# Kernel tuning notes

Measured on AMD Instinct MI355X. Metric: run time of the kernel, lower is better.

Reference implementation:

```python
import jax, jax.numpy as jnp
import numpy as np

N = 50000      # nodes
E = 800000     # edges
IN = 128       # in_dim
EMB = 32       # emb_dim
ED = 8         # edge_dim
L = 4          # num_layers
B = 64         # num graphs in batch
OUT = 10       # out_dim
EPS = 1e-5


def setup_inputs() -> dict:
    key = jax.random.key(0)
    ks = jax.random.split(key, 16)
    f32 = jnp.float32
    def nrm(k, shape, scale):
        return jax.random.normal(k, shape, dtype=f32) * scale
    inp = {}
    inp['x'] = nrm(ks[0], (N, IN), 1.0)
    inp['edge_index'] = jax.random.randint(ks[1], (2, E), 0, N)
    inp['edge_attr'] = nrm(ks[2], (E, ED), 1.0)
    inp['batch'] = jnp.sort(jax.random.randint(ks[3], (N,), 0, B))
    # lin_in
    inp['lin_in_w'] = nrm(ks[4], (IN, EMB), 0.05)
    inp['lin_in_b'] = jnp.zeros((EMB,), f32)
    # per-layer message MLP: Linear(2e+ed->e), BN, ReLU, Linear(e->e), BN, ReLU
    inp['msg_w1'] = nrm(ks[5], (L, 2 * EMB + ED, EMB), 0.1)
    inp['msg_b1'] = jnp.zeros((L, EMB), f32)
    inp['msg_g1'] = jnp.ones((L, EMB), f32)
    inp['msg_be1'] = jnp.zeros((L, EMB), f32)
    inp['msg_w2'] = nrm(ks[6], (L, EMB, EMB), 0.1)
    inp['msg_b2'] = jnp.zeros((L, EMB), f32)
    inp['msg_g2'] = jnp.ones((L, EMB), f32)
    inp['msg_be2'] = jnp.zeros((L, EMB), f32)
    # per-layer update MLP: Linear(2e->e), BN, ReLU, Linear(e->e), BN, ReLU
    inp['upd_w1'] = nrm(ks[7], (L, 2 * EMB, EMB), 0.1)
    inp['upd_b1'] = jnp.zeros((L, EMB), f32)
    inp['upd_g1'] = jnp.ones((L, EMB), f32)
    inp['upd_be1'] = jnp.zeros((L, EMB), f32)
    inp['upd_w2'] = nrm(ks[8], (L, EMB, EMB), 0.1)
    inp['upd_b2'] = jnp.zeros((L, EMB), f32)
    inp['upd_g2'] = jnp.ones((L, EMB), f32)
    inp['upd_be2'] = jnp.zeros((L, EMB), f32)
    # lin_pred
    inp['pred_w'] = nrm(ks[9], (EMB, OUT), 0.1)
    inp['pred_b'] = jnp.zeros((OUT,), f32)
    return inp


def _bn(x, g, b):
    # BatchNorm1d in training mode: batch stats over dim 0 (biased variance)
    mu = jnp.mean(x, axis=0)
    var = jnp.mean(jnp.square(x - mu), axis=0)
    return (x - mu) * jax.lax.rsqrt(var + EPS) * g + b


def reference(x, edge_attr, lin_in_w, lin_in_b,
              msg_w1, msg_b1, msg_g1, msg_be1, msg_w2, msg_b2, msg_g2, msg_be2,
              upd_w1, upd_b1, upd_g1, upd_be1, upd_w2, upd_b2, upd_g2, upd_be2,
              pred_w, pred_b, edge_index, batch):
    src = edge_index[0]  # h_j source nodes
    dst = edge_index[1]  # h_i target nodes (aggregation index)
    h = x @ lin_in_w + lin_in_b  # [N, EMB]
    for i in range(L):
        # message: gather + concat + MLP(BN,ReLU)x2 over edges
        msg_in = jnp.concatenate([h[dst], h[src], edge_attr], axis=-1)  # [E, 2e+ed]
        m = jax.nn.relu(_bn(msg_in @ msg_w1[i] + msg_b1[i], msg_g1[i], msg_be1[i]))
        m = jax.nn.relu(_bn(m @ msg_w2[i] + msg_b2[i], msg_g2[i], msg_be2[i]))
        # aggregate: scatter-add by destination
        aggr = jax.ops.segment_sum(m, dst, num_segments=N)  # [N, EMB]
        # update: concat + MLP(BN,ReLU)x2
        u = jnp.concatenate([h, aggr], axis=-1)  # [N, 2e]
        u = jax.nn.relu(_bn(u @ upd_w1[i] + upd_b1[i], upd_g1[i], upd_be1[i]))
        u = jax.nn.relu(_bn(u @ upd_w2[i] + upd_b2[i], upd_g2[i], upd_be2[i]))
        h = u + h  # residual in MPNNModel.get_embeddings
    # global mean pool
    sums = jax.ops.segment_sum(h, batch, num_segments=B)
    counts = jax.ops.segment_sum(jnp.ones((N,), h.dtype), batch, num_segments=B)
    h_graph = sums / jnp.maximum(counts, 1.0)[:, None]
    return h_graph @ pred_w + pred_b  # [B, OUT]
```

## Files before the change

### kernel.cpp

```cpp
#include <hip/hip_runtime.h>
#include <cstddef>

#define N_NODES 50000
#define N_EDGES 800000
#define IN_DIM  128
#define EMB     32
#define ED      8
#define NLAYERS 4
#define NB      64
#define OUTD    10
#define EPS_BN  1e-5f

#define EDGE_GRID 3125
#define NODE_GRID 196
#define NODE4_GRID 782
#define AU_GRID   6250
#define NT16      50000
#define NTILE_N   3125
#define LIN_GRID  782
#define MSG2_TPW  16
#define MSG2_GRID 782

#define SREP 4

typedef short bf16x8 __attribute__((ext_vector_type(8)));
typedef float f32x4  __attribute__((ext_vector_type(4)));


__device__ __forceinline__ unsigned short f2bf(float x) {
  union { float f; unsigned u; } v; v.f = x;
  unsigned b = v.u + 0x7FFFu + ((v.u >> 16) & 1u);
  return (unsigned short)(b >> 16);
}
__device__ __forceinline__ float bf2f(unsigned short s) {
  union { unsigned u; float f; } v; v.u = ((unsigned)s) << 16;
  return v.f;
}

__device__ __forceinline__ void coef_from_stats(const float* __restrict__ stats_stage,
                                                const float* __restrict__ g,
                                                const float* __restrict__ be,
                                                float inv_count, float* __restrict__ cf) {
  if (threadIdx.x < EMB) {
    const int c = threadIdx.x;
    float s = 0.f, ss = 0.f;
#pragma unroll
    for (int r = 0; r < SREP; ++r) {
      s  += stats_stage[r*64 + c];
      ss += stats_stage[r*64 + EMB + c];
    }
    const float mu  = s * inv_count;
    const float var = ss * inv_count - mu*mu;
    const float a = g[c] * rsqrtf(var + EPS_BN);
    cf[c] = a;
    cf[EMB + c] = fmaf(-mu, a, be[c]);
  }
  __syncthreads();
}

__device__ __forceinline__ void wave_stats_atomic(float ts[8], float tss[8],
                                                  float* __restrict__ lds_s,
                                                  float* __restrict__ lds_q,
                                                  float* __restrict__ stats_stage) {
  const int lane = threadIdx.x & 63;
  const int wv   = threadIdx.x >> 6;
#pragma unroll
  for (int j = 0; j < 8; ++j) {
    float a = ts[j], b = tss[j];
#pragma unroll
    for (int o = 32; o > 0; o >>= 1) {
      a += __shfl_down(a, o, 64);
      b += __shfl_down(b, o, 64);
    }
    ts[j] = a; tss[j] = b;
  }
  if (lane == 0) {
#pragma unroll
    for (int j = 0; j < 8; ++j) {
      lds_s[wv*8 + j] = ts[j];
      lds_q[wv*8 + j] = tss[j];
    }
  }
  __syncthreads();
  if (threadIdx.x < 64) {
    const float v = (threadIdx.x < 32) ? lds_s[threadIdx.x] : lds_q[threadIdx.x - 32];
    atomicAdd(stats_stage + ((blockIdx.x & (SREP-1)) << 6) + threadIdx.x, v);
  }
}

__device__ __forceinline__ void half_stats_atomic(const float ts[16], const float tss[16],
                                                  float* __restrict__ stats_stage) {
  __shared__ float s_s[4][32], s_q[4][32];
  const int lane = threadIdx.x & 63;
  const int wid  = threadIdx.x >> 6;
#pragma unroll
  for (int j = 0; j < 16; ++j) {
    float a = ts[j], q = tss[j];
#pragma unroll
    for (int o = 32; o >= 2; o >>= 1) {
      a += __shfl_down(a, o, 64);
      q += __shfl_down(q, o, 64);
    }
    if (lane < 2) { s_s[wid][lane*16 + j] = a; s_q[wid][lane*16 + j] = q; }
  }
  __syncthreads();
  if (threadIdx.x < 64) {
    const int c = threadIdx.x & 31;
    const int kind = threadIdx.x >> 5;
    float v = 0.f;
#pragma unroll
    for (int wq = 0; wq < 4; ++wq)
      v += kind ? s_q[wq][c] : s_s[wq][c];
    atomicAdd(stats_stage + ((blockIdx.x & (SREP-1)) << 6) + kind*32 + c, v);
  }
}

#define HSTRIDE 40

__global__ __launch_bounds__(256) void k_lin_in_pq(
    const float* __restrict__ x, const float* __restrict__ w, const float* __restrict__ b,
    const float* __restrict__ w1, const float* __restrict__ b1, const int* __restrict__ ei,
    float* __restrict__ h, unsigned short* __restrict__ p, unsigned short* __restrict__ q,
    int* __restrict__ cnt)
{
  __shared__ __align__(16) unsigned short lds_hb[4][16*HSTRIDE];
  __shared__ __align__(16) unsigned short lds_pq[4][16*HSTRIDE];
  const int lane = threadIdx.x & 63;
  const int wv   = threadIdx.x >> 6;
  const int n0i  = lane & 15;
  const int quad = lane >> 4;

  const int tile = blockIdx.x*4 + wv;
  if (tile < NTILE_N) {
    const int r0 = tile*16;
    bf16x8 BwL[4], BwH[4];
#pragma unroll
    for (int kb = 0; kb < 4; ++kb) {
#pragma unroll
      for (int j = 0; j < 8; ++j) {
        const int k = kb*32 + quad*8 + j;
        BwL[kb][j] = (short)f2bf(w[k*EMB + n0i]);
        BwH[kb][j] = (short)f2bf(w[k*EMB + 16 + n0i]);
      }
    }
    f32x4 accL = {0.f,0.f,0.f,0.f};
    f32x4 accH = {0.f,0.f,0.f,0.f};
#pragma unroll
    for (int kb = 0; kb < 4; ++kb) {
      const float4 xa = *(const float4*)(x + (size_t)(r0 + n0i)*IN_DIM + kb*32 + quad*8);
      const float4 xb = *(const float4*)(x + (size_t)(r0 + n0i)*IN_DIM + kb*32 + quad*8 + 4);
      bf16x8 A;
      A[0] = (short)f2bf(xa.x); A[1] = (short)f2bf(xa.y);
      A[2] = (short)f2bf(xa.z); A[3] = (short)f2bf(xa.w);
      A[4] = (short)f2bf(xb.x); A[5] = (short)f2bf(xb.y);
      A[6] = (short)f2bf(xb.z); A[7] = (short)f2bf(xb.w);
      accL = __builtin_amdgcn_mfma_f32_16x16x32_bf16(A, BwL[kb], accL, 0, 0, 0);
      accH = __builtin_amdgcn_mfma_f32_16x16x32_bf16(A, BwH[kb], accH, 0, 0, 0);
    }
    const float bL = b[n0i], bH = b[16 + n0i];
#pragma unroll
    for (int r = 0; r < 4; ++r) {
      const int row = quad*4 + r;
      const float vL = accL[r] + bL;
      const float vH = accH[r] + bH;
      h[(size_t)(r0 + row)*EMB + n0i]      = vL;
      h[(size_t)(r0 + row)*EMB + 16 + n0i] = vH;
      lds_hb[wv][row*HSTRIDE + n0i]      = f2bf(vL);
      lds_hb[wv][row*HSTRIDE + 16 + n0i] = f2bf(vH);
    }
    bf16x8 A2;
#pragma unroll
    for (int j = 0; j < 8; ++j)
      A2[j] = (short)lds_hb[wv][n0i*HSTRIDE + quad*8 + j];
    bf16x8 BpL, BpH, BqL, BqH;
#pragma unroll
    for (int j = 0; j < 8; ++j) {
      const int k = quad*8 + j;
      BpL[j] = (short)f2bf(w1[k*EMB + n0i]);
      BpH[j] = (short)f2bf(w1[k*EMB + 16 + n0i]);
      BqL[j] = (short)f2bf(w1[(EMB + k)*EMB + n0i]);
      BqH[j] = (short)f2bf(w1[(EMB + k)*EMB + 16 + n0i]);
    }
    const f32x4 z4 = {0.f,0.f,0.f,0.f};
    f32x4 pL = __builtin_amdgcn_mfma_f32_16x16x32_bf16(A2, BpL, z4, 0, 0, 0);
    f32x4 pH = __builtin_amdgcn_mfma_f32_16x16x32_bf16(A2, BpH, z4, 0, 0, 0);
    f32x4 qL = __builtin_amdgcn_mfma_f32_16x16x32_bf16(A2, BqL, z4, 0, 0, 0);
    f32x4 qH = __builtin_amdgcn_mfma_f32_16x16x32_bf16(A2, BqH, z4, 0, 0, 0);
    const float b1L = b1[n0i], b1H = b1[16 + n0i];
#pragma unroll
    for (int r = 0; r < 4; ++r) {
      const int row = quad*4 + r;
      lds_pq[wv][row*HSTRIDE + n0i]      = f2bf(pL[r] + b1L);
      lds_pq[wv][row*HSTRIDE + 16 + n0i] = f2bf(pH[r] + b1H);
    }
    {
      const int row2 = lane >> 2;
      const int c8   = (lane & 3)*8;
      const uint4 ov = *(const uint4*)&lds_pq[wv][row2*HSTRIDE + c8];
      *(uint4*)(p + (size_t)(r0 + row2)*EMB + c8) = ov;
    }
#pragma unroll
    for (int r = 0; r < 4; ++r) {
      const int row = quad*4 + r;
      lds_pq[wv][row*HSTRIDE + n0i]      = f2bf(qL[r]);
      lds_pq[wv][row*HSTRIDE + 16 + n0i] = f2bf(qH[r]);
    }
    {
      const int row2 = lane >> 2;
      const int c8   = (lane & 3)*8;
      const uint4 ov = *(const uint4*)&lds_pq[wv][row2*HSTRIDE + c8];
      *(uint4*)(q + (size_t)(r0 + row2)*EMB + c8) = ov;
    }
  }
  for (int e = blockIdx.x*256 + threadIdx.x; e < N_EDGES; e += gridDim.x*256)
    atomicAdd(&cnt[ei[N_EDGES + e]], 1);
}

__global__ __launch_bounds__(256) void k_scan_a(const int* __restrict__ cnt,
                                                int* __restrict__ row_ptr, int* __restrict__ bsum) {
  __shared__ int s[256];
  const int gid = blockIdx.x*256 + threadIdx.x;
  const int v = (gid < N_NODES) ? cnt[gid] : 0;
  s[threadIdx.x] = v;
  __syncthreads();
  for (int o = 1; o < 256; o <<= 1) {
    const int t = (threadIdx.x >= o) ? s[threadIdx.x - o] : 0;
    __syncthreads();
    s[threadIdx.x] += t;
    __syncthreads();
  }
  if (gid < N_NODES) row_ptr[gid] = s[threadIdx.x] - v;
  if (threadIdx.x == 255) bsum[blockIdx.x] = s[255];
}

__global__ __launch_bounds__(256) void k_scan_bc(int* __restrict__ row_ptr,
                                                 const int* __restrict__ bsum) {
  __shared__ int s[256];
  const int t = threadIdx.x;
  const int v = (t < NODE_GRID) ? bsum[t] : 0;
  s[t] = v;
  __syncthreads();
  for (int o = 1; o < 256; o <<= 1) {
    const int tt = (t >= o) ? s[t - o] : 0;
    __syncthreads();
    s[t] += tt;
    __syncthreads();
  }
  const int off = (blockIdx.x == 0) ? 0 : s[blockIdx.x - 1];
  const int gid = blockIdx.x*256 + t;
  if (gid < N_NODES) row_ptr[gid] += off;
  if (blockIdx.x == 0 && t == 0) row_ptr[N_NODES] = N_EDGES;
}

__global__ __launch_bounds__(256) void k_place_scatter(
    const int* __restrict__ ei, const float* __restrict__ ea,
    const int* __restrict__ row_ptr, int* __restrict__ cnt2,
    uint2* __restrict__ rec)
{
  const int e = blockIdx.x*256 + threadIdx.x;
  const int s = ei[e];
  const int d = ei[N_EDGES + e];
  const int pos = row_ptr[d] + atomicAdd(&cnt2[d], 1);
  const float4 v0 = ((const float4*)(ea + (size_t)e*ED))[0];
  const float4 v1 = ((const float4*)(ea + (size_t)e*ED))[1];
  const float ev[8] = {v0.x, v0.y, v0.z, v0.w, v1.x, v1.y, v1.z, v1.w};
  unsigned u[4];
#pragma unroll
  for (int j = 0; j < 4; ++j)
    u[j] = (unsigned)f2bf(ev[2*j]) | ((unsigned)f2bf(ev[2*j+1]) << 16);
  uint2* rp = rec + (size_t)pos*3;
  rp[0] = make_uint2((unsigned)s, (unsigned)d);
  rp[1] = make_uint2(u[0], u[1]);
  rp[2] = make_uint2(u[2], u[3]);
}


__device__ __forceinline__ void msg1_edge(const uint4 Pa, const uint4 Pb,
                                          const uint4 Qa, const uint4 Qb,
                                          const uint2 rb, const uint2 rc,
                                          const float* __restrict__ wh,
                                          float acc[16])
{
  const unsigned pw[8] = {Pa.x,Pa.y,Pa.z,Pa.w,Pb.x,Pb.y,Pb.z,Pb.w};
  const unsigned qw[8] = {Qa.x,Qa.y,Qa.z,Qa.w,Qb.x,Qb.y,Qb.z,Qb.w};
#pragma unroll
  for (int t = 0; t < 8; ++t) {
    acc[2*t]   = bf2f((unsigned short)(pw[t] & 0xFFFFu)) +
                 bf2f((unsigned short)(qw[t] & 0xFFFFu));
    acc[2*t+1] = bf2f((unsigned short)(pw[t] >> 16)) +
                 bf2f((unsigned short)(qw[t] >> 16));
  }
  const unsigned ew[4] = {rb.x, rb.y, rc.x, rc.y};
  float ev[8];
#pragma unroll
  for (int t = 0; t < 4; ++t) {
    ev[2*t]   = bf2f((unsigned short)(ew[t] & 0xFFFFu));
    ev[2*t+1] = bf2f((unsigned short)(ew[t] >> 16));
  }
#pragma unroll
  for (int k = 0; k < 8; ++k) {
    const float* wk = wh + k*EMB;
#pragma unroll
    for (int j = 0; j < 16; ++j) acc[j] = fmaf(ev[k], wk[j], acc[j]);
  }
}

__device__ __forceinline__ void msg1_store_stats(const float acc[16],
                                                 unsigned short* __restrict__ dst,
                                                 float ts[16], float tss[16])
{
  unsigned u[8];
#pragma unroll
  for (int j = 0; j < 8; ++j) {
    const unsigned short l0 = f2bf(acc[2*j]);
    const unsigned short h0 = f2bf(acc[2*j+1]);
    u[j] = (unsigned)l0 | ((unsigned)h0 << 16);
    const float v0 = bf2f(l0), v1 = bf2f(h0);
    ts[2*j]   += v0; tss[2*j]   = fmaf(v0, v0, tss[2*j]);
    ts[2*j+1] += v1; tss[2*j+1] = fmaf(v1, v1, tss[2*j+1]);
  }
  uint4 o0; o0.x = u[0]; o0.y = u[1]; o0.z = u[2]; o0.w = u[3];
  uint4 o1; o1.x = u[4]; o1.y = u[5]; o1.z = u[6]; o1.w = u[7];
  ((uint4*)dst)[0] = o0;
  ((uint4*)dst)[1] = o1;
}

__global__ __launch_bounds__(256) void k_msg1(
    const unsigned short* __restrict__ pb, const unsigned short* __restrict__ qb,
    const uint2* __restrict__ rec, const float* __restrict__ w1b,
    unsigned short* __restrict__ y, float* __restrict__ stats)
{
  const int t    = threadIdx.x;
  const int half = t & 1;
  const int eh   = t >> 1;
  const int e0   = blockIdx.x*256 + eh;
  const int e1   = e0 + 128;

  const uint2 r0a = rec[(size_t)e0*3];
  const uint2 r0b = rec[(size_t)e0*3 + 1];
  const uint2 r0c = rec[(size_t)e0*3 + 2];
  const uint2 r1a = rec[(size_t)e1*3];
  const uint2 r1b = rec[(size_t)e1*3 + 1];
  const uint2 r1c = rec[(size_t)e1*3 + 2];

  const uint4* p0 = (const uint4*)(pb + (size_t)r0a.y * EMB) + half*2;
  const uint4* q0 = (const uint4*)(qb + (size_t)r0a.x * EMB) + half*2;
  const uint4* p1 = (const uint4*)(pb + (size_t)r1a.y * EMB) + half*2;
  const uint4* q1 = (const uint4*)(qb + (size_t)r1a.x * EMB) + half*2;
  const uint4 P0a = p0[0], P0b = p0[1];
  const uint4 Q0a = q0[0], Q0b = q0[1];
  const uint4 P1a = p1[0], P1b = p1[1];
  const uint4 Q1a = q1[0], Q1b = q1[1];

  const float* wh = w1b + half*16;

  float ts[16], tss[16];
#pragma unroll
  for (int j = 0; j < 16; ++j) { ts[j] = 0.f; tss[j] = 0.f; }

  float acc[16];
  msg1_edge(P0a, P0b, Q0a, Q0b, r0b, r0c, wh, acc);
  msg1_store_stats(acc, y + (size_t)e0*EMB + half*16, ts, tss);
  msg1_edge(P1a, P1b, Q1a, Q1b, r1b, r1c, wh, acc);
  msg1_store_stats(acc, y + (size_t)e1*EMB + half*16, ts, tss);

  half_stats_atomic(ts, tss, stats);
}

__global__ __launch_bounds__(256) void k_msg2(
    unsigned short* __restrict__ y,
    const float* __restrict__ stats1, const float* __restrict__ g1, const float* __restrict__ be1,
    const float* __restrict__ w2, const float* __restrict__ b2,
    float* __restrict__ stats2)
{
  __shared__ __align__(16) unsigned short lds_t[4][16*32];
  __shared__ float lds_s[4][32], lds_q[4][32];
  __shared__ float cf[64];

  coef_from_stats(stats1, g1, be1, 1.0f/(float)N_EDGES, cf);

  const int lane = threadIdx.x & 63;
  const int wid  = threadIdx.x >> 6;
  const int n0 = lane & 15;
  const int kb = lane >> 4;

  bf16x8 Blo, Bhi;
#pragma unroll
  for (int j = 0; j < 8; ++j) {
    Blo[j] = (short)f2bf(w2[(kb*8 + j)*EMB + n0]);
    Bhi[j] = (short)f2bf(w2[(kb*8 + j)*EMB + 16 + n0]);
  }
  float a1[8], c1[8];
#pragma unroll
  for (int j = 0; j < 8; ++j) {
    a1[j] = cf[kb*8 + j];
    c1[j] = cf[EMB + kb*8 + j];
  }
  const float b2c0 = b2[n0], b2c1 = b2[16 + n0];

  float ts[8], tss[8];
#pragma unroll
  for (int j = 0; j < 8; ++j) { ts[j] = 0.f; tss[j] = 0.f; }

  const int tile0 = blockIdx.x * (MSG2_TPW*4);
  for (int t = 0; t < MSG2_TPW; ++t) {
    const int tile = tile0 + t*4 + wid;
    if (tile >= NT16) break;
    const size_t e0 = (size_t)tile * 16;

    const uint4 araw = *(const uint4*)(y + (e0 + n0)*EMB + kb*8);
    unsigned int ua[4] = {araw.x, araw.y, araw.z, araw.w};
    bf16x8 A;
#pragma unroll
    for (int j = 0; j < 4; ++j) {
      float v0 = bf2f((unsigned short)(ua[j] & 0xFFFFu));
      float v1 = bf2f((unsigned short)(ua[j] >> 16));
      v0 = fmaxf(fmaf(a1[2*j],   v0, c1[2*j]),   0.f);
      v1 = fmaxf(fmaf(a1[2*j+1], v1, c1[2*j+1]), 0.f);
      A[2*j]   = (short)f2bf(v0);
      A[2*j+1] = (short)f2bf(v1);
    }

    f32x4 acc0 = {0.f, 0.f, 0.f, 0.f};
    f32x4 acc1 = {0.f, 0.f, 0.f, 0.f};
    acc0 = __builtin_amdgcn_mfma_f32_16x16x32_bf16(A, Blo, acc0, 0, 0, 0);
    acc1 = __builtin_amdgcn_mfma_f32_16x16x32_bf16(A, Bhi, acc1, 0, 0, 0);

#pragma unroll
    for (int r = 0; r < 4; ++r) {
      const int row = kb*4 + r;
      lds_t[wid][row*32 + n0]      = f2bf(acc0[r] + b2c0);
      lds_t[wid][row*32 + 16 + n0] = f2bf(acc1[r] + b2c1);
    }
    const uint4 orow = *(const uint4*)&lds_t[wid][(lane>>2)*32 + (lane&3)*8];
    *(uint4*)(y + (e0 + (lane>>2))*EMB + (lane&3)*8) = orow;

    unsigned int uo[4] = {orow.x, orow.y, orow.z, orow.w};
#pragma unroll
    for (int j = 0; j < 4; ++j) {
      const float v0 = bf2f((unsigned short)(uo[j] & 0xFFFFu));
      const float v1 = bf2f((unsigned short)(uo[j] >> 16));
      ts[2*j]   += v0;  tss[2*j]   = fmaf(v0, v0, tss[2*j]);
      ts[2*j+1] += v1;  tss[2*j+1] = fmaf(v1, v1, tss[2*j+1]);
    }
  }

#pragma unroll
  for (int j = 0; j < 8; ++j) {
    float s = ts[j], qq = tss[j];
#pragma unroll
    for (int o = 4; o < 64; o <<= 1) {
      s  += __shfl_xor(s, o, 64);
      qq += __shfl_xor(qq, o, 64);
    }
    ts[j] = s; tss[j] = qq;
  }
  if (lane < 4) {
#pragma unroll
    for (int j = 0; j < 8; ++j) {
      lds_s[wid][lane*8 + j] = ts[j];
      lds_q[wid][lane*8 + j] = tss[j];
    }
  }
  __syncthreads();
  if (threadIdx.x < 64) {
    const int c = threadIdx.x & 31;
    const int kind = threadIdx.x >> 5;
    float v = 0.f;
#pragma unroll
    for (int wq = 0; wq < 4; ++wq)
      v += kind ? lds_q[wq][c] : lds_s[wq][c];
    atomicAdd(stats2 + ((blockIdx.x & (SREP-1)) << 6) + kind*32 + c, v);
  }
}

__global__ __launch_bounds__(256) void k_aggr_upd1(
    const unsigned short* __restrict__ y, const int* __restrict__ row_ptr,
    const float* __restrict__ h,
    const float* __restrict__ stats1, const float* __restrict__ g2, const float* __restrict__ be2,
    const float* __restrict__ uw1, const float* __restrict__ ub1,
    float* __restrict__ z, float* __restrict__ stats2)
{
  __shared__ float cf[64];
  __shared__ float lh[8][32];
  __shared__ float la[8][32];
  __shared__ float rs[4][32], rq[4][32];
  coef_from_stats(stats1, g2, be2, 1.0f/(float)N_EDGES, cf);

  const int g = threadIdx.x >> 5;
  const int l = threadIdx.x & 31;
  const int n = blockIdx.x*8 + g;

  lh[g][l] = h[(size_t)n*EMB + l];

  const int rof = l >> 4;
  const int cp  = l & 15;
  const float a0 = cf[2*cp],     b0 = cf[EMB + 2*cp];
  const float a1 = cf[2*cp + 1], b1 = cf[EMB + 2*cp + 1];
  const int lo = row_ptr[n], hi = row_ptr[n+1];
  float s0 = 0.f, s1 = 0.f;
  for (int i = lo + rof; i < hi; i += 2) {
    const unsigned u = *(const unsigned*)(y + (size_t)i*EMB + 2*cp);
    const float v0 = bf2f((unsigned short)(u & 0xFFFFu));
    const float v1 = bf2f((unsigned short)(u >> 16));
    s0 += fmaxf(fmaf(a0, v0, b0), 0.f);
    s1 += fmaxf(fmaf(a1, v1, b1), 0.f);
  }
  s0 += __shfl_xor(s0, 16, 64);
  s1 += __shfl_xor(s1, 16, 64);
  if (rof == 0) { la[g][2*cp] = s0; la[g][2*cp + 1] = s1; }
  __syncthreads();

  float acc = ub1[l];
#pragma unroll
  for (int k = 0; k < EMB; ++k) acc = fmaf(lh[g][k], uw1[k*EMB + l], acc);
#pragma unroll
  for (int k = 0; k < EMB; ++k) acc = fmaf(la[g][k], uw1[(EMB + k)*EMB + l], acc);
  z[(size_t)n*EMB + l] = acc;

  const float sq = acc*acc;
  const float a2 = acc + __shfl_down(acc, 32, 64);
  const float q2 = sq  + __shfl_down(sq,  32, 64);
  const int wv = threadIdx.x >> 6;
  if ((threadIdx.x & 63) < 32) { rs[wv][l] = a2; rq[wv][l] = q2; }
  __syncthreads();
  if (threadIdx.x < 64) {
    const int c = threadIdx.x & 31;
    const int kind = threadIdx.x >> 5;
    float v = 0.f;
#pragma unroll
    for (int wq = 0; wq < 4; ++wq)
      v += kind ? rq[wq][c] : rs[wq][c];
    atomicAdd(stats2 + ((blockIdx.x & (SREP-1)) << 6) + kind*32 + c, v);
  }
}

__global__ __launch_bounds__(256) void k_upd2(
    float* __restrict__ z,
    const float* __restrict__ stats1, const float* __restrict__ g1, const float* __restrict__ be1,
    const float* __restrict__ w, const float* __restrict__ b,
    float* __restrict__ stats2)
{
  __shared__ float cf[64];
  __shared__ float lds_s[32], lds_q[32];
  coef_from_stats(stats1, g1, be1, 1.0f/(float)N_NODES, cf);

  const int lane = threadIdx.x & 63;
  const int wv   = threadIdx.x >> 6;
  const int n  = blockIdx.x*64 + lane;
  const int c0 = wv*8;
  float acc[8];
#pragma unroll
  for (int j = 0; j < 8; ++j) acc[j] = 0.f;
  if (n < N_NODES) {
#pragma unroll
    for (int j = 0; j < 8; ++j) acc[j] = b[c0 + j];
    const float4* zp = (const float4*)(z + (size_t)n*EMB);
#pragma unroll
    for (int k4 = 0; k4 < 8; ++k4) {
      const float4 v = zp[k4];
      const float mv[4] = {v.x, v.y, v.z, v.w};
#pragma unroll
      for (int t = 0; t < 4; ++t) {
        const int k = 4*k4 + t;
        const float m = fmaxf(fmaf(cf[k], mv[t], cf[EMB + k]), 0.f);
        const float* wk = w + k*EMB + c0;
#pragma unroll
        for (int j = 0; j < 8; ++j) acc[j] = fmaf(m, wk[j], acc[j]);
      }
    }
  }
  float ts[8], tss[8];
#pragma unroll
  for (int j = 0; j < 8; ++j) { ts[j] = acc[j]; tss[j] = acc[j]*acc[j]; }
  wave_stats_atomic(ts, tss, lds_s, lds_q, stats2);
  if (n < N_NODES) {
    float4 o0, o1;
    o0.x = acc[0]; o0.y = acc[1]; o0.z = acc[2]; o0.w = acc[3];
    o1.x = acc[4]; o1.y = acc[5]; o1.z = acc[6]; o1.w = acc[7];
    *(float4*)(z + (size_t)n*EMB + c0)     = o0;
    *(float4*)(z + (size_t)n*EMB + c0 + 4) = o1;
  }
}

__global__ __launch_bounds__(256) void k_resid_pq(
    float* __restrict__ h, const float* __restrict__ z,
    const float* __restrict__ stats, const float* __restrict__ g, const float* __restrict__ be,
    const float* __restrict__ w1_next, const float* __restrict__ b1_next,
    unsigned short* __restrict__ p, unsigned short* __restrict__ q)
{
  __shared__ float cf[64];
  __shared__ float lds_h[64][33];
  coef_from_stats(stats, g, be, 1.0f/(float)N_NODES, cf);

  const int lane = threadIdx.x & 63;
  const int wv   = threadIdx.x >> 6;
  const int n  = blockIdx.x*64 + lane;
  const int c0 = wv*8;
  if (n < N_NODES) {
    const float4* zp = (const float4*)(z + (size_t)n*EMB + c0);
    float4* hp = (float4*)(h + (size_t)n*EMB + c0);
    float hn[8];
    const float4 z0 = zp[0], z1 = zp[1];
    const float4 h0 = hp[0], h1 = hp[1];
    const float zv[8] = {z0.x, z0.y, z0.z, z0.w, z1.x, z1.y, z1.z, z1.w};
    const float hv[8] = {h0.x, h0.y, h0.z, h0.w, h1.x, h1.y, h1.z, h1.w};
#pragma unroll
    for (int j = 0; j < 8; ++j) {
      const int k = c0 + j;
      hn[j] = hv[j] + fmaxf(fmaf(cf[k], zv[j], cf[EMB + k]), 0.f);
      lds_h[lane][k] = hn[j];
    }
    float4 o0, o1;
    o0.x = hn[0]; o0.y = hn[1]; o0.z = hn[2]; o0.w = hn[3];
    o1.x = hn[4]; o1.y = hn[5]; o1.z = hn[6]; o1.w = hn[7];
    hp[0] = o0; hp[1] = o1;
  }
  __syncthreads();
  if (n < N_NODES && w1_next) {
    float ap[8], aq[8];
#pragma unroll
    for (int j = 0; j < 8; ++j) { ap[j] = b1_next[c0 + j]; aq[j] = 0.f; }
#pragma unroll
    for (int k = 0; k < EMB; ++k) {
      const float hvv = lds_h[lane][k];
      const float* wp = w1_next + k*EMB + c0;
      const float* wq = w1_next + (EMB + k)*EMB + c0;
#pragma unroll
      for (int j = 0; j < 8; ++j) ap[j] = fmaf(hvv, wp[j], ap[j]);
#pragma unroll
      for (int j = 0; j < 8; ++j) aq[j] = fmaf(hvv, wq[j], aq[j]);
    }
    unsigned up[4], uq[4];
#pragma unroll
    for (int j = 0; j < 4; ++j) {
      up[j] = (unsigned)f2bf(ap[2*j]) | ((unsigned)f2bf(ap[2*j+1]) << 16);
      uq[j] = (unsigned)f2bf(aq[2*j]) | ((unsigned)f2bf(aq[2*j+1]) << 16);
    }
    uint4 op; op.x = up[0]; op.y = up[1]; op.z = up[2]; op.w = up[3];
    uint4 oq; oq.x = uq[0]; oq.y = uq[1]; oq.z = uq[2]; oq.w = uq[3];
    *(uint4*)(p + (size_t)n*EMB + c0) = op;
    *(uint4*)(q + (size_t)n*EMB + c0) = oq;
  }
}

__global__ void k_pool(const float* __restrict__ h, const int* __restrict__ batch,
                       const float* __restrict__ pw, const float* __restrict__ pb,
                       float* __restrict__ out)
{
  __shared__ float sred[256];
  __shared__ float hg[EMB];
  const int b = blockIdx.x;
  int lo = 0, hi = N_NODES;
  while (lo < hi) { int m = (lo + hi) >> 1; if (batch[m] < b) lo = m + 1; else hi = m; }
  const int start = lo;
  hi = N_NODES;
  while (lo < hi) { int m = (lo + hi) >> 1; if (batch[m] < b + 1) lo = m + 1; else hi = m; }
  const int end = lo;

  const int c = threadIdx.x & (EMB-1);
  const int r = threadIdx.x >> 5;
  float s = 0.f;
  for (int n = start + r; n < end; n += 8) s += h[(size_t)n*EMB + c];
  sred[threadIdx.x] = s;
  __syncthreads();
  if (threadIdx.x < EMB) {
    float tot = 0.f;
#pragma unroll
    for (int r2 = 0; r2 < 8; ++r2) tot += sred[r2*EMB + threadIdx.x];
    const float cnt = (float)(end - start);
    hg[threadIdx.x] = tot / fmaxf(cnt, 1.f);
  }
  __syncthreads();
  if (threadIdx.x < OUTD) {
    float acc = pb[threadIdx.x];
#pragma unroll
    for (int cc = 0; cc < EMB; ++cc) acc = fmaf(hg[cc], pw[cc*OUTD + threadIdx.x], acc);
    out[b*OUTD + threadIdx.x] = acc;
  }
}


extern "C" void kernel_launch(void* const* d_in, const int* in_sizes, int n_in,
                              void* d_out, int out_size, void* d_ws, size_t ws_size,
                              hipStream_t stream) {
  const float* x        = (const float*)d_in[0];
  const int*   ei       = (const int*)  d_in[1];
  const float* ea       = (const float*)d_in[2];
  const int*   batch    = (const int*)  d_in[3];
  const float* lin_in_w = (const float*)d_in[4];
  const float* lin_in_b = (const float*)d_in[5];
  const float* msg_w1   = (const float*)d_in[6];
  const float* msg_b1   = (const float*)d_in[7];
  const float* msg_g1   = (const float*)d_in[8];
  const float* msg_be1  = (const float*)d_in[9];
  const float* msg_w2   = (const float*)d_in[10];
  const float* msg_b2   = (const float*)d_in[11];
  const float* msg_g2   = (const float*)d_in[12];
  const float* msg_be2  = (const float*)d_in[13];
  const float* upd_w1   = (const float*)d_in[14];
  const float* upd_b1   = (const float*)d_in[15];
  const float* upd_g1   = (const float*)d_in[16];
  const float* upd_be1  = (const float*)d_in[17];
  const float* upd_w2   = (const float*)d_in[18];
  const float* upd_b2   = (const float*)d_in[19];
  const float* upd_g2   = (const float*)d_in[20];
  const float* upd_be2  = (const float*)d_in[21];
  const float* pred_w   = (const float*)d_in[22];
  const float* pred_b   = (const float*)d_in[23];
  float* out = (float*)d_out;

  char* wsb = (char*)d_ws;
  unsigned short* y  = (unsigned short*)wsb;
  uint2* rec = (uint2*)(wsb + (size_t)N_EDGES*EMB*2);
  unsigned short* p  = (unsigned short*)(rec + (size_t)N_EDGES*3);
  unsigned short* q  = p + (size_t)N_NODES*EMB;
  float* h       = (float*)(q + (size_t)N_NODES*EMB);
  float* z       = h + (size_t)N_NODES*EMB;
  float* stats   = z + (size_t)N_NODES*EMB;
  int*   cnt     = (int*)(stats + 16*SREP*64);
  int*   cnt2    = cnt + N_NODES;
  int*   row_ptr = cnt2 + N_NODES;
  int*   bsum    = row_ptr + N_NODES + 1;
  const size_t need = ((size_t)((char*)(bsum + 256) - wsb));
  if (ws_size < need) return;

  hipMemsetAsync(stats, 0, (16*SREP*64 + 2*N_NODES)*sizeof(float), stream);

  k_lin_in_pq<<<LIN_GRID, 256, 0, stream>>>(x, lin_in_w, lin_in_b, msg_w1, msg_b1, ei,
                                            h, p, q, cnt);
  k_scan_a<<<NODE_GRID, 256, 0, stream>>>(cnt, row_ptr, bsum);
  k_scan_bc<<<NODE_GRID, 256, 0, stream>>>(row_ptr, bsum);
  k_place_scatter<<<EDGE_GRID, 256, 0, stream>>>(ei, ea, row_ptr, cnt2, rec);

  for (int l = 0; l < NLAYERS; ++l) {
    const int st = l*4;
    const float* w1  = msg_w1 + (size_t)l*(2*EMB+ED)*EMB;
    const float* w1b = w1 + (size_t)2*EMB*EMB;
    const float* w2  = msg_w2 + (size_t)l*EMB*EMB;
    const float* uw1 = upd_w1 + (size_t)l*(2*EMB)*EMB;
    const float* uw2 = upd_w2 + (size_t)l*EMB*EMB;
    const float* w1_next = (l+1 < NLAYERS) ? msg_w1 + (size_t)(l+1)*(2*EMB+ED)*EMB : nullptr;
    const float* b1_next = (l+1 < NLAYERS) ? msg_b1 + (size_t)(l+1)*EMB : nullptr;

    k_msg1<<<EDGE_GRID, 256, 0, stream>>>(p, q, rec, w1b, y, stats + (size_t)st*SREP*64);
    k_msg2<<<MSG2_GRID, 256, 0, stream>>>(y, stats + (size_t)st*SREP*64,
                                          msg_g1 + l*EMB, msg_be1 + l*EMB,
                                          w2, msg_b2 + l*EMB, stats + (size_t)(st+1)*SREP*64);
    k_aggr_upd1<<<AU_GRID, 256, 0, stream>>>(y, row_ptr, h,
                                             stats + (size_t)(st+1)*SREP*64,
                                             msg_g2 + l*EMB, msg_be2 + l*EMB,
                                             uw1, upd_b1 + l*EMB,
                                             z, stats + (size_t)(st+2)*SREP*64);
    k_upd2<<<NODE4_GRID, 256, 0, stream>>>(z, stats + (size_t)(st+2)*SREP*64,
                                           upd_g1 + l*EMB, upd_be1 + l*EMB,
                                           uw2, upd_b2 + l*EMB, stats + (size_t)(st+3)*SREP*64);
    k_resid_pq<<<NODE4_GRID, 256, 0, stream>>>(h, z, stats + (size_t)(st+3)*SREP*64,
                                               upd_g2 + l*EMB, upd_be2 + l*EMB,
                                               w1_next, b1_next, p, q);
  }

  k_pool<<<NB, 256, 0, stream>>>(h, batch, pred_w, pred_b, out);
}
```

Baseline: 905.3 us.

## Recompute first message layer in msg2 instead of storing it, using MFMA

New measurement: 847.8 us. 1.07x faster.

```diff
diff --git a/kernel.cpp b/kernel.cpp
--- a/kernel.cpp
+++ b/kernel.cpp
@@ -15,11 +15,12 @@
 #define NODE_GRID 196
 #define NODE4_GRID 782
 #define AU_GRID   6250
-#define NT16      50000
 #define NTILE_N   3125
 #define LIN_GRID  782
-#define MSG2_TPW  16
-#define MSG2_GRID 782
+#define ST_TPW    4
+#define ST_GRID   3125
+#define MSG2_TPW  4
+#define MSG2_GRID 3125
 
 #define SREP 4
 
@@ -85,33 +86,6 @@
   if (threadIdx.x < 64) {
     const float v = (threadIdx.x < 32) ? lds_s[threadIdx.x] : lds_q[threadIdx.x - 32];
     atomicAdd(stats_stage + ((blockIdx.x & (SREP-1)) << 6) + threadIdx.x, v);
-  }
-}
-
-__device__ __forceinline__ void half_stats_atomic(const float ts[16], const float tss[16],
-                                                  float* __restrict__ stats_stage) {
-  __shared__ float s_s[4][32], s_q[4][32];
-  const int lane = threadIdx.x & 63;
-  const int wid  = threadIdx.x >> 6;
-#pragma unroll
-  for (int j = 0; j < 16; ++j) {
-    float a = ts[j], q = tss[j];
-#pragma unroll
-    for (int o = 32; o >= 2; o >>= 1) {
-      a += __shfl_down(a, o, 64);
-      q += __shfl_down(q, o, 64);
-    }
-    if (lane < 2) { s_s[wid][lane*16 + j] = a; s_q[wid][lane*16 + j] = q; }
-  }
-  __syncthreads();
-  if (threadIdx.x < 64) {
-    const int c = threadIdx.x & 31;
-    const int kind = threadIdx.x >> 5;
-    float v = 0.f;
-#pragma unroll
-    for (int wq = 0; wq < 4; ++wq)
-      v += kind ? s_q[wq][c] : s_s[wq][c];
-    atomicAdd(stats_stage + ((blockIdx.x & (SREP-1)) << 6) + kind*32 + c, v);
   }
 }
 
@@ -275,104 +249,112 @@
 }
 
 
-__device__ __forceinline__ void msg1_edge(const uint4 Pa, const uint4 Pb,
-                                          const uint4 Qa, const uint4 Qb,
-                                          const uint2 rb, const uint2 rc,
-                                          const float* __restrict__ wh,
-                                          float acc[16])
-{
-  const unsigned pw[8] = {Pa.x,Pa.y,Pa.z,Pa.w,Pb.x,Pb.y,Pb.z,Pb.w};
-  const unsigned qw[8] = {Qa.x,Qa.y,Qa.z,Qa.w,Qb.x,Qb.y,Qb.z,Qb.w};
-#pragma unroll
-  for (int t = 0; t < 8; ++t) {
-    acc[2*t]   = bf2f((unsigned short)(pw[t] & 0xFFFFu)) +
-                 bf2f((unsigned short)(qw[t] & 0xFFFFu));
-    acc[2*t+1] = bf2f((unsigned short)(pw[t] >> 16)) +
-                 bf2f((unsigned short)(qw[t] >> 16));
-  }
-  const unsigned ew[4] = {rb.x, rb.y, rc.x, rc.y};
-  float ev[8];
-#pragma unroll
-  for (int t = 0; t < 4; ++t) {
-    ev[2*t]   = bf2f((unsigned short)(ew[t] & 0xFFFFu));
-    ev[2*t+1] = bf2f((unsigned short)(ew[t] >> 16));
-  }
-#pragma unroll
-  for (int k = 0; k < 8; ++k) {
-    const float* wk = wh + k*EMB;
-#pragma unroll
-    for (int j = 0; j < 16; ++j) acc[j] = fmaf(ev[k], wk[j], acc[j]);
-  }
-}
-
-__device__ __forceinline__ void msg1_store_stats(const float acc[16],
-                                                 unsigned short* __restrict__ dst,
-                                                 float ts[16], float tss[16])
-{
-  unsigned u[8];
-#pragma unroll
-  for (int j = 0; j < 8; ++j) {
-    const unsigned short l0 = f2bf(acc[2*j]);
-    const unsigned short h0 = f2bf(acc[2*j+1]);
-    u[j] = (unsigned)l0 | ((unsigned)h0 << 16);
-    const float v0 = bf2f(l0), v1 = bf2f(h0);
-    ts[2*j]   += v0; tss[2*j]   = fmaf(v0, v0, tss[2*j]);
-    ts[2*j+1] += v1; tss[2*j+1] = fmaf(v1, v1, tss[2*j+1]);
-  }
-  uint4 o0; o0.x = u[0]; o0.y = u[1]; o0.z = u[2]; o0.w = u[3];
-  uint4 o1; o1.x = u[4]; o1.y = u[5]; o1.z = u[6]; o1.w = u[7];
-  ((uint4*)dst)[0] = o0;
-  ((uint4*)dst)[1] = o1;
-}
-
-__global__ __launch_bounds__(256) void k_msg1(
+__global__ __launch_bounds__(256) void k_stats1(
     const unsigned short* __restrict__ pb, const unsigned short* __restrict__ qb,
     const uint2* __restrict__ rec, const float* __restrict__ w1b,
-    unsigned short* __restrict__ y, float* __restrict__ stats)
+    float* __restrict__ stats)
 {
-  const int t    = threadIdx.x;
-  const int half = t & 1;
-  const int eh   = t >> 1;
-  const int e0   = blockIdx.x*256 + eh;
-  const int e1   = e0 + 128;
-
-  const uint2 r0a = rec[(size_t)e0*3];
-  const uint2 r0b = rec[(size_t)e0*3 + 1];
-  const uint2 r0c = rec[(size_t)e0*3 + 2];
-  const uint2 r1a = rec[(size_t)e1*3];
-  const uint2 r1b = rec[(size_t)e1*3 + 1];
-  const uint2 r1c = rec[(size_t)e1*3 + 2];
-
-  const uint4* p0 = (const uint4*)(pb + (size_t)r0a.y * EMB) + half*2;
-  const uint4* q0 = (const uint4*)(qb + (size_t)r0a.x * EMB) + half*2;
-  const uint4* p1 = (const uint4*)(pb + (size_t)r1a.y * EMB) + half*2;
-  const uint4* q1 = (const uint4*)(qb + (size_t)r1a.x * EMB) + half*2;
-  const uint4 P0a = p0[0], P0b = p0[1];
-  const uint4 Q0a = q0[0], Q0b = q0[1];
-  const uint4 P1a = p1[0], P1b = p1[1];
-  const uint4 Q1a = q1[0], Q1b = q1[1];
-
-  const float* wh = w1b + half*16;
-
-  float ts[16], tss[16];
-#pragma unroll
-  for (int j = 0; j < 16; ++j) { ts[j] = 0.f; tss[j] = 0.f; }
-
-  float acc[16];
-  msg1_edge(P0a, P0b, Q0a, Q0b, r0b, r0c, wh, acc);
-  msg1_store_stats(acc, y + (size_t)e0*EMB + half*16, ts, tss);
-  msg1_edge(P1a, P1b, Q1a, Q1b, r1b, r1c, wh, acc);
-  msg1_store_stats(acc, y + (size_t)e1*EMB + half*16, ts, tss);
-
-  half_stats_atomic(ts, tss, stats);
+  __shared__ float lds_d[4][16*33];
+  __shared__ float lds_s[4][32], lds_q[4][32];
+  const int lane = threadIdx.x & 63;
+  const int wv   = threadIdx.x >> 6;
+  const int l15  = lane & 15;
+  const int quad = lane >> 4;
+
+  bf16x8 B1lo = {}, B1hi = {};
+  if (quad == 0) {
+#pragma unroll
+    for (int j = 0; j < 8; ++j) {
+      B1lo[j] = (short)f2bf(w1b[j*EMB + l15]);
+      B1hi[j] = (short)f2bf(w1b[j*EMB + 16 + l15]);
+    }
+  }
+
+  float ts[8], tss[8];
+#pragma unroll
+  for (int j = 0; j < 8; ++j) { ts[j] = 0.f; tss[j] = 0.f; }
+
+  const int tile0 = blockIdx.x * (4*ST_TPW);
+#pragma unroll
+  for (int t = 0; t < ST_TPW; ++t) {
+    const int tile = tile0 + t*4 + wv;
+    const size_t e0 = (size_t)tile * 16;
+
+    bf16x8 A = {};
+    if (quad == 0) {
+      const uint2 rb = rec[(e0 + l15)*3 + 1];
+      const uint2 rc = rec[(e0 + l15)*3 + 2];
+      A[0] = (short)(rb.x & 0xFFFFu); A[1] = (short)(rb.x >> 16);
+      A[2] = (short)(rb.y & 0xFFFFu); A[3] = (short)(rb.y >> 16);
+      A[4] = (short)(rc.x & 0xFFFFu); A[5] = (short)(rc.x >> 16);
+      A[6] = (short)(rc.y & 0xFFFFu); A[7] = (short)(rc.y >> 16);
+    }
+    const f32x4 z4 = {0.f,0.f,0.f,0.f};
+    f32x4 D0 = __builtin_amdgcn_mfma_f32_16x16x32_bf16(A, B1lo, z4, 0, 0, 0);
+    f32x4 D1 = __builtin_amdgcn_mfma_f32_16x16x32_bf16(A, B1hi, z4, 0, 0, 0);
+#pragma unroll
+    for (int r = 0; r < 4; ++r) {
+      const int row = quad*4 + r;
+      lds_d[wv][row*33 + l15]      = D0[r];
+      lds_d[wv][row*33 + 16 + l15] = D1[r];
+    }
+    const uint2 sd = rec[(e0 + l15)*3];
+    const uint4 pg = *(const uint4*)(pb + (size_t)sd.y*EMB + quad*8);
+    const uint4 qg = *(const uint4*)(qb + (size_t)sd.x*EMB + quad*8);
+    const unsigned pu[4] = {pg.x, pg.y, pg.z, pg.w};
+    const unsigned qu[4] = {qg.x, qg.y, qg.z, qg.w};
+#pragma unroll
+    for (int jj = 0; jj < 4; ++jj) {
+      const float d0 = lds_d[wv][l15*33 + quad*8 + 2*jj];
+      const float d1 = lds_d[wv][l15*33 + quad*8 + 2*jj + 1];
+      const float v0 = (d0 + bf2f((unsigned short)(pu[jj] & 0xFFFFu)))
+                            + bf2f((unsigned short)(qu[jj] & 0xFFFFu));
+      const float v1 = (d1 + bf2f((unsigned short)(pu[jj] >> 16)))
+                            + bf2f((unsigned short)(qu[jj] >> 16));
+      const float w0 = bf2f(f2bf(v0));
+      const float w1v = bf2f(f2bf(v1));
+      ts[2*jj]   += w0;  tss[2*jj]   = fmaf(w0, w0, tss[2*jj]);
+      ts[2*jj+1] += w1v; tss[2*jj+1] = fmaf(w1v, w1v, tss[2*jj+1]);
+    }
+  }
+
+#pragma unroll
+  for (int j = 0; j < 8; ++j) {
+    float a = ts[j], b = tss[j];
+#pragma unroll
+    for (int o = 1; o < 16; o <<= 1) {
+      a += __shfl_xor(a, o, 64);
+      b += __shfl_xor(b, o, 64);
+    }
+    ts[j] = a; tss[j] = b;
+  }
+  if (l15 == 0) {
+#pragma unroll
+    for (int j = 0; j < 8; ++j) {
+      lds_s[wv][quad*8 + j] = ts[j];
+      lds_q[wv][quad*8 + j] = tss[j];
+    }
+  }
+  __syncthreads();
+  if (threadIdx.x < 64) {
+    const int c = threadIdx.x & 31;
+    const int kind = threadIdx.x >> 5;
+    float v = 0.f;
+#pragma unroll
+    for (int wq = 0; wq < 4; ++wq)
+      v += kind ? lds_q[wq][c] : lds_s[wq][c];
+    atomicAdd(stats + ((blockIdx.x & (SREP-1)) << 6) + kind*32 + c, v);
+  }
 }
 
 __global__ __launch_bounds__(256) void k_msg2(
-    unsigned short* __restrict__ y,
+    const unsigned short* __restrict__ pb, const unsigned short* __restrict__ qb,
+    const uint2* __restrict__ rec, const float* __restrict__ w1b,
     const float* __restrict__ stats1, const float* __restrict__ g1, const float* __restrict__ be1,
     const float* __restrict__ w2, const float* __restrict__ b2,
-    float* __restrict__ stats2)
+    unsigned short* __restrict__ y, float* __restrict__ stats2)
 {
+  __shared__ float lds_d[4][16*33];
   __shared__ __align__(16) unsigned short lds_t[4][16*32];
   __shared__ float lds_s[4][32], lds_q[4][32];
   __shared__ float cf[64];
@@ -380,62 +362,97 @@
   coef_from_stats(stats1, g1, be1, 1.0f/(float)N_EDGES, cf);
 
   const int lane = threadIdx.x & 63;
-  const int wid  = threadIdx.x >> 6;
-  const int n0 = lane & 15;
-  const int kb = lane >> 4;
-
+  const int wv   = threadIdx.x >> 6;
+  const int l15  = lane & 15;
+  const int quad = lane >> 4;
+
+  bf16x8 B1lo = {}, B1hi = {};
+  if (quad == 0) {
+#pragma unroll
+    for (int j = 0; j < 8; ++j) {
+      B1lo[j] = (short)f2bf(w1b[j*EMB + l15]);
+      B1hi[j] = (short)f2bf(w1b[j*EMB + 16 + l15]);
+    }
+  }
   bf16x8 Blo, Bhi;
 #pragma unroll
   for (int j = 0; j < 8; ++j) {
-    Blo[j] = (short)f2bf(w2[(kb*8 + j)*EMB + n0]);
-    Bhi[j] = (short)f2bf(w2[(kb*8 + j)*EMB + 16 + n0]);
+    Blo[j] = (short)f2bf(w2[(quad*8 + j)*EMB + l15]);
+    Bhi[j] = (short)f2bf(w2[(quad*8 + j)*EMB + 16 + l15]);
   }
   float a1[8], c1[8];
 #pragma unroll
   for (int j = 0; j < 8; ++j) {
-    a1[j] = cf[kb*8 + j];
-    c1[j] = cf[EMB + kb*8 + j];
-  }
-  const float b2c0 = b2[n0], b2c1 = b2[16 + n0];
+    a1[j] = cf[quad*8 + j];
+    c1[j] = cf[EMB + quad*8 + j];
+  }
+  const float b2c0 = b2[l15], b2c1 = b2[16 + l15];
 
   float ts[8], tss[8];
 #pragma unroll
   for (int j = 0; j < 8; ++j) { ts[j] = 0.f; tss[j] = 0.f; }
 
-  const int tile0 = blockIdx.x * (MSG2_TPW*4);
+  const int tile0 = blockIdx.x * (4*MSG2_TPW);
+#pragma unroll
   for (int t = 0; t < MSG2_TPW; ++t) {
-    const int tile = tile0 + t*4 + wid;
-    if (tile >= NT16) break;
+    const int tile = tile0 + t*4 + wv;
     const size_t e0 = (size_t)tile * 16;
 
-    const uint4 araw = *(const uint4*)(y + (e0 + n0)*EMB + kb*8);
-    unsigned int ua[4] = {araw.x, araw.y, araw.z, araw.w};
-    bf16x8 A;
-#pragma unroll
-    for (int j = 0; j < 4; ++j) {
-      float v0 = bf2f((unsigned short)(ua[j] & 0xFFFFu));
-      float v1 = bf2f((unsigned short)(ua[j] >> 16));
-      v0 = fmaxf(fmaf(a1[2*j],   v0, c1[2*j]),   0.f);
-      v1 = fmaxf(fmaf(a1[2*j+1], v1, c1[2*j+1]), 0.f);
-      A[2*j]   = (short)f2bf(v0);
-      A[2*j+1] = (short)f2bf(v1);
+    bf16x8 A = {};
+    if (quad == 0) {
+      const uint2 rb = rec[(e0 + l15)*3 + 1];
+      const uint2 rc = rec[(e0 + l15)*3 + 2];
+      A[0] = (short)(rb.x & 0xFFFFu); A[1] = (short)(rb.x >> 16);
+      A[2] = (short)(rb.y & 0xFFFFu); A[3] = (short)(rb.y >> 16);
+      A[4] = (short)(rc.x & 0xFFFFu); A[5] = (short)(rc.x >> 16);
+      A[6] = (short)(rc.y & 0xFFFFu); A[7] = (short)(rc.y >> 16);
+    }
+    const f32x4 z4 = {0.f,0.f,0.f,0.f};
+    f32x4 D0 = __builtin_amdgcn_mfma_f32_16x16x32_bf16(A, B1lo, z4, 0, 0, 0);
+    f32x4 D1 = __builtin_amdgcn_mfma_f32_16x16x32_bf16(A, B1hi, z4, 0, 0, 0);
+#pragma unroll
+    for (int r = 0; r < 4; ++r) {
+      const int row = quad*4 + r;
+      lds_d[wv][row*33 + l15]      = D0[r];
+      lds_d[wv][row*33 + 16 + l15] = D1[r];
+    }
+    const uint2 sd = rec[(e0 + l15)*3];
+    const uint4 pg = *(const uint4*)(pb + (size_t)sd.y*EMB + quad*8);
+    const uint4 qg = *(const uint4*)(qb + (size_t)sd.x*EMB + quad*8);
+    const unsigned pu[4] = {pg.x, pg.y, pg.z, pg.w};
+    const unsigned qu[4] = {qg.x, qg.y, qg.z, qg.w};
+    bf16x8 A2;
+#pragma unroll
+    for (int jj = 0; jj < 4; ++jj) {
+      const float d0 = lds_d[wv][l15*33 + quad*8 + 2*jj];
+      const float d1 = lds_d[wv][l15*33 + quad*8 + 2*jj + 1];
+      const float v0 = (d0 + bf2f((unsigned short)(pu[jj] & 0xFFFFu)))
+                            + bf2f((unsigned short)(qu[jj] & 0xFFFFu));
+      const float v1 = (d1 + bf2f((unsigned short)(pu[jj] >> 16)))
+                            + bf2f((unsigned short)(qu[jj] >> 16));
+      const float w0 = bf2f(f2bf(v0));
+      const float w1v = bf2f(f2bf(v1));
+      const float r0 = fmaxf(fmaf(a1[2*jj],   w0,  c1[2*jj]),   0.f);
+      const float r1 = fmaxf(fmaf(a1[2*jj+1], w1v, c1[2*jj+1]), 0.f);
+      A2[2*jj]   = (short)f2bf(r0);
+      A2[2*jj+1] = (short)f2bf(r1);
     }
 
     f32x4 acc0 = {0.f, 0.f, 0.f, 0.f};
     f32x4 acc1 = {0.f, 0.f, 0.f, 0.f};
-    acc0 = __builtin_amdgcn_mfma_f32_16x16x32_bf16(A, Blo, acc0, 0, 0, 0);
-    acc1 = __builtin_amdgcn_mfma_f32_16x16x32_bf16(A, Bhi, acc1, 0, 0, 0);
+    acc0 = __builtin_amdgcn_mfma_f32_16x16x32_bf16(A2, Blo, acc0, 0, 0, 0);
+    acc1 = __builtin_amdgcn_mfma_f32_16x16x32_bf16(A2, Bhi, acc1, 0, 0, 0);
 
 #pragma unroll
     for (int r = 0; r < 4; ++r) {
-      const int row = kb*4 + r;
-      lds_t[wid][row*32 + n0]      = f2bf(acc0[r] + b2c0);
-      lds_t[wid][row*32 + 16 + n0] = f2bf(acc1[r] + b2c1);
-    }
-    const uint4 orow = *(const uint4*)&lds_t[wid][(lane>>2)*32 + (lane&3)*8];
+      const int row = quad*4 + r;
+      lds_t[wv][row*32 + l15]      = f2bf(acc0[r] + b2c0);
+      lds_t[wv][row*32 + 16 + l15] = f2bf(acc1[r] + b2c1);
+    }
+    const uint4 orow = *(const uint4*)&lds_t[wv][(lane>>2)*32 + (lane&3)*8];
     *(uint4*)(y + (e0 + (lane>>2))*EMB + (lane&3)*8) = orow;
 
-    unsigned int uo[4] = {orow.x, orow.y, orow.z, orow.w};
+    const unsigned uo[4] = {orow.x, orow.y, orow.z, orow.w};
 #pragma unroll
     for (int j = 0; j < 4; ++j) {
       const float v0 = bf2f((unsigned short)(uo[j] & 0xFFFFu));
@@ -458,8 +475,8 @@
   if (lane < 4) {
 #pragma unroll
     for (int j = 0; j < 8; ++j) {
-      lds_s[wid][lane*8 + j] = ts[j];
-      lds_q[wid][lane*8 + j] = tss[j];
+      lds_s[wv][lane*8 + j] = ts[j];
+      lds_q[wv][lane*8 + j] = tss[j];
     }
   }
   __syncthreads();
@@ -743,10 +760,12 @@
     const float* w1_next = (l+1 < NLAYERS) ? msg_w1 + (size_t)(l+1)*(2*EMB+ED)*EMB : nullptr;
     const float* b1_next = (l+1 < NLAYERS) ? msg_b1 + (size_t)(l+1)*EMB : nullptr;
 
-    k_msg1<<<EDGE_GRID, 256, 0, stream>>>(p, q, rec, w1b, y, stats + (size_t)st*SREP*64);
-    k_msg2<<<MSG2_GRID, 256, 0, stream>>>(y, stats + (size_t)st*SREP*64,
+    k_stats1<<<ST_GRID, 256, 0, stream>>>(p, q, rec, w1b, stats + (size_t)st*SREP*64);
+    k_msg2<<<MSG2_GRID, 256, 0, stream>>>(p, q, rec, w1b,
+                                          stats + (size_t)st*SREP*64,
                                           msg_g1 + l*EMB, msg_be1 + l*EMB,
-                                          w2, msg_b2 + l*EMB, stats + (size_t)(st+1)*SREP*64);
+                                          w2, msg_b2 + l*EMB,
+                                          y, stats + (size_t)(st+1)*SREP*64);
     k_aggr_upd1<<<AU_GRID, 256, 0, stream>>>(y, row_ptr, h,
                                              stats + (size_t)(st+1)*SREP*64,
                                              msg_g2 + l*EMB, msg_be2 + l*EMB,
```
